# Performance work log

Measured on AMD Instinct MI355X. Metric: run time of the kernel, lower is better.

Reference implementation:

```python
import jax, jax.numpy as jnp
import numpy as np

B, IN, H, N, W, K = 32, 256, 512, 32768, 64, 8
EPS = 1e-12  # torch F.normalize eps


def setup_inputs() -> dict:
    key = jax.random.key(0)
    ks = jax.random.split(key, 16)
    inp = {
        "x": jax.random.normal(ks[0], (B, IN), jnp.float32),
        "h_prev": jax.random.normal(ks[1], (B, H), jnp.float32),
        "c_prev": jax.random.normal(ks[2], (B, H), jnp.float32),
        "M_prev": jax.random.normal(ks[3], (B, N, W), jnp.float32),
        "wr_prev": jax.random.uniform(ks[4], (B, N), jnp.float32),
        "usage_prev": jax.random.uniform(ks[5], (B, N), jnp.float32),
        "r_prev": jax.random.normal(ks[6], (B, W), jnp.float32),
        # LSTMCell params (torch layout: [4H, in] / [4H, H], gate order i,f,g,o)
        "W_ih": jax.random.normal(ks[7], (4 * H, IN + W), jnp.float32) * 0.02,
        "W_hh": jax.random.normal(ks[8], (4 * H, H), jnp.float32) * 0.02,
        "b_ih": jax.random.normal(ks[9], (4 * H,), jnp.float32) * 0.02,
        "b_hh": jax.random.normal(ks[10], (4 * H,), jnp.float32) * 0.02,
        # output_projector: hidden -> 3W + 2
        "W_proj": jax.random.normal(ks[11], (3 * W + 2, H), jnp.float32) * 0.02,
        "b_proj": jax.random.normal(ks[12], (3 * W + 2,), jnp.float32) * 0.02,
        # final_projector: hidden + W -> hidden
        "W_final": jax.random.normal(ks[13], (H, H + W), jnp.float32) * 0.02,
        "b_final": jax.random.normal(ks[14], (H,), jnp.float32) * 0.02,
    }
    return inp


def _l2norm(v, axis):
    n = jnp.sqrt(jnp.sum(v * v, axis=axis, keepdims=True))
    return v / jnp.maximum(n, EPS)


def reference(x, h_prev, c_prev, M_prev, wr_prev, usage_prev, r_prev,
              W_ih, W_hh, b_ih, b_hh, W_proj, b_proj, W_final, b_final):
    # ---- LSTM controller step ----
    lstm_in = jnp.concatenate([x, r_prev], axis=1)            # [B, IN+W]
    gates = lstm_in @ W_ih.T + b_ih + h_prev @ W_hh.T + b_hh  # [B, 4H]
    gi, gf, gg, go = jnp.split(gates, 4, axis=1)
    i = jax.nn.sigmoid(gi)
    f = jax.nn.sigmoid(gf)
    g = jnp.tanh(gg)
    o = jax.nn.sigmoid(go)
    c_curr = f * c_prev + i * g
    h_curr = o * jnp.tanh(c_curr)

    # ---- interface params ----
    params = h_curr @ W_proj.T + b_proj                       # [B, 3W+2]
    q = params[:, :W]
    a = params[:, W:2 * W]
    e = jax.nn.sigmoid(params[:, 2 * W:3 * W])
    alpha = jax.nn.sigmoid(params[:, -2:-1])                  # [B,1]
    gamma = jax.nn.sigmoid(params[:, -1:])                    # [B,1]

    # ---- sparse read: cosine sim -> topK -> scattered softmax ----
    q_n = _l2norm(q, axis=1)                                  # [B, W]
    m_n = _l2norm(M_prev, axis=2)                             # [B, N, W]
    sim = jnp.einsum('bw,bnw->bn', q_n, m_n)                  # [B, N]
    top_vals, top_idx = jax.lax.top_k(sim, K)                 # [B, K]
    sm = jax.nn.softmax(top_vals, axis=1)                     # softmax(-inf elsewhere) == 0
    b_idx = jnp.arange(sim.shape[0])[:, None]
    w_r = jnp.zeros_like(sim).at[b_idx, top_idx].set(sm)      # [B, N]
    r_curr = jnp.einsum('bn,bnw->bw', w_r, M_prev)            # [B, W]

    # ---- usage / LRU write weights ----
    usage_curr = usage_prev + 1.0
    access_mask = jnp.zeros_like(usage_curr).at[b_idx, top_idx].set(1.0)
    usage_curr = usage_curr * (1.0 - access_mask)
    lru = jnp.argmax(usage_curr, axis=1)                      # [B]
    I_U = jax.nn.one_hot(lru, usage_curr.shape[1], dtype=usage_curr.dtype)
    w_w = alpha * (gamma * wr_prev + (1.0 - gamma) * I_U)     # [B, N]

    # ---- rank-1 erase / add memory update ----
    w_w_exp = w_w[:, :, None]                                 # [B, N, 1]
    M_curr = M_prev * (1.0 - w_w_exp * e[:, None, :]) + w_w_exp * a[:, None, :]

    # ---- output ----
    y_out = jnp.concatenate([h_curr, r_curr], axis=1) @ W_final.T + b_final
    return (y_out, h_curr, c_curr, M_curr, w_r, usage_curr, r_curr)
```

## Files before the change

kernel.cpp:

```cpp
#include <hip/hip_runtime.h>
#include <math.h>

#define B_ 32
#define IN_ 256
#define H_ 512
#define N_ 32768
#define W_ 64
#define K_ 8
#define PROJ_ 194
#define NCHUNK 32
#define CROWS 1024
#define NCAND 1024

typedef float f32x4 __attribute__((ext_vector_type(4)));

#define OUT_Y  0
#define OUT_H  16384
#define OUT_C  32768
#define OUT_M  49152
#define OUT_WR 67158016
#define OUT_US 68206592
#define OUT_R  69255168

#define WS_QN    0
#define WS_AA    2048
#define WS_EE    4096
#define WS_ALPHA 6144
#define WS_GAMMA 6176
#define WS_LRU   6208
#define WS_CVAL  8192
#define WS_CIDX  40960

__device__ __forceinline__ float sigmoidf_(float v) { return 1.f / (1.f + expf(-v)); }

__global__ __launch_bounds__(256) void k_lstm(
    const float* __restrict__ x, const float* __restrict__ r_prev,
    const float* __restrict__ h_prev, const float* __restrict__ c_prev,
    const float* __restrict__ W_ih, const float* __restrict__ W_hh,
    const float* __restrict__ b_ih, const float* __restrict__ b_hh,
    float* __restrict__ h_out, float* __restrict__ c_out) {
  int wid = (blockIdx.x * blockDim.x + threadIdx.x) >> 6;
  int lane = threadIdx.x & 63;
  if (wid >= B_ * H_) return;
  int b = wid >> 9;
  int h = wid & (H_ - 1);
  float a0 = 0.f, a1 = 0.f, a2 = 0.f, a3 = 0.f;
  const float4* x4 = (const float4*)(x + b * IN_);
  const float4* r4 = (const float4*)(r_prev + b * W_);
  for (int c = lane; c < 80; c += 64) {
    float4 in4 = (c < 64) ? x4[c] : r4[c - 64];
    #pragma unroll
    for (int g = 0; g < 4; ++g) {
      float4 w4 = ((const float4*)(W_ih + (size_t)(g * H_ + h) * 320))[c];
      float d = fmaf(w4.x, in4.x, fmaf(w4.y, in4.y, fmaf(w4.z, in4.z, w4.w * in4.w)));
      if (g == 0) a0 += d; else if (g == 1) a1 += d; else if (g == 2) a2 += d; else a3 += d;
    }
  }
  const float4* h4 = (const float4*)(h_prev + b * H_);
  for (int c = lane; c < 128; c += 64) {
    float4 in4 = h4[c];
    #pragma unroll
    for (int g = 0; g < 4; ++g) {
      float4 w4 = ((const float4*)(W_hh + (size_t)(g * H_ + h) * 512))[c];
      float d = fmaf(w4.x, in4.x, fmaf(w4.y, in4.y, fmaf(w4.z, in4.z, w4.w * in4.w)));
      if (g == 0) a0 += d; else if (g == 1) a1 += d; else if (g == 2) a2 += d; else a3 += d;
    }
  }
  #pragma unroll
  for (int m = 1; m < 64; m <<= 1) {
    a0 += __shfl_xor(a0, m); a1 += __shfl_xor(a1, m);
    a2 += __shfl_xor(a2, m); a3 += __shfl_xor(a3, m);
  }
  if (lane == 0) {
    float gi = a0 + b_ih[h] + b_hh[h];
    float gf = a1 + b_ih[H_ + h] + b_hh[H_ + h];
    float gg = a2 + b_ih[2 * H_ + h] + b_hh[2 * H_ + h];
    float go = a3 + b_ih[3 * H_ + h] + b_hh[3 * H_ + h];
    float i_ = sigmoidf_(gi), f_ = sigmoidf_(gf), g_ = tanhf(gg), o_ = sigmoidf_(go);
    float cc = f_ * c_prev[b * H_ + h] + i_ * g_;
    c_out[b * H_ + h] = cc;
    h_out[b * H_ + h] = o_ * tanhf(cc);
  }
}

__global__ __launch_bounds__(256) void k_projpost(
    const float* __restrict__ h_curr, const float* __restrict__ W_proj,
    const float* __restrict__ b_proj, float* __restrict__ qn,
    float* __restrict__ aa, float* __restrict__ ee,
    float* __restrict__ alpha, float* __restrict__ gamma) {
  int b = blockIdx.x, tid = threadIdx.x;
  int wave = tid >> 6, lane = tid & 63;
  __shared__ float params[PROJ_];
  const float4* h4 = (const float4*)(h_curr + b * H_);
  float4 ha = h4[lane], hb = h4[lane + 64];
  for (int p = wave; p < PROJ_; p += 4) {
    const float4* w4p = (const float4*)(W_proj + (size_t)p * H_);
    float4 wa = w4p[lane], wb = w4p[lane + 64];
    float acc = fmaf(wa.x, ha.x, fmaf(wa.y, ha.y, fmaf(wa.z, ha.z, wa.w * ha.w)))
              + fmaf(wb.x, hb.x, fmaf(wb.y, hb.y, fmaf(wb.z, hb.z, wb.w * hb.w)));
    #pragma unroll
    for (int m = 1; m < 64; m <<= 1) acc += __shfl_xor(acc, m);
    if (lane == 0) params[p] = acc + b_proj[p];
  }
  __syncthreads();
  if (tid < W_) {
    float q = params[tid];
    float s = q * q;
    #pragma unroll
    for (int m = 1; m < 64; m <<= 1) s += __shfl_xor(s, m);
    float nrm = fmaxf(sqrtf(s), 1e-12f);
    qn[b * W_ + tid] = q / nrm;
    aa[b * W_ + tid] = params[W_ + tid];
    ee[b * W_ + tid] = sigmoidf_(params[2 * W_ + tid]);
    if (tid == 0) alpha[b] = sigmoidf_(params[192]);
    if (tid == 1) gamma[b] = sigmoidf_(params[193]);
  }
}

__global__ __launch_bounds__(256) void k_simupd(
    const float* __restrict__ M, const float* __restrict__ qn,
    const float* __restrict__ wr_prev, const float* __restrict__ aa,
    const float* __restrict__ ee, const float* __restrict__ alpha,
    const float* __restrict__ gamma, float* __restrict__ M_out,
    float* __restrict__ cval, int* __restrict__ cidx, float* __restrict__ w_r) {
  int b = blockIdx.y, chunk = blockIdx.x, tid = threadIdx.x;
  int j = tid & 15;
  __shared__ float simv[CROWS];
  f32x4 z = {0.f, 0.f, 0.f, 0.f};
  __builtin_nontemporal_store(z, (f32x4*)(w_r + (size_t)b * N_ + chunk * CROWS + tid * 4));
  const float* Mb = M + ((size_t)b * N_ + (size_t)chunk * CROWS) * W_;
  float* Ob = M_out + ((size_t)b * N_ + (size_t)chunk * CROWS) * W_;
  const float* wrb = wr_prev + (size_t)b * N_ + chunk * CROWS;
  float4 q4 = ((const float4*)(qn + b * W_))[j];
  float4 e4 = ((const float4*)(ee + b * W_))[j];
  float4 a4 = ((const float4*)(aa + b * W_))[j];
  float c0 = alpha[b] * gamma[b];
  #pragma unroll 8
  for (int it = 0; it < 64; ++it) {
    float4 m4 = *(const float4*)(Mb + (size_t)it * 1024 + tid * 4);
    int r = it * 16 + (tid >> 4);
    float ww = c0 * wrb[r];
    f32x4 o;
    o.x = fmaf(m4.x, 1.f - ww * e4.x, ww * a4.x);
    o.y = fmaf(m4.y, 1.f - ww * e4.y, ww * a4.y);
    o.z = fmaf(m4.z, 1.f - ww * e4.z, ww * a4.z);
    o.w = fmaf(m4.w, 1.f - ww * e4.w, ww * a4.w);
    __builtin_nontemporal_store(o, (f32x4*)(Ob + (size_t)it * 1024 + tid * 4));
    float dot = fmaf(m4.x, q4.x, fmaf(m4.y, q4.y, fmaf(m4.z, q4.z, m4.w * q4.w)));
    float sq  = fmaf(m4.x, m4.x, fmaf(m4.y, m4.y, fmaf(m4.z, m4.z, m4.w * m4.w)));
    #pragma unroll
    for (int m = 1; m < 16; m <<= 1) { dot += __shfl_xor(dot, m); sq += __shfl_xor(sq, m); }
    if (j == 0) simv[r] = dot / fmaxf(sqrtf(sq), 1e-12f);
  }
  __syncthreads();
  int wave = tid >> 6, lane = tid & 63;
  int rbase = wave * 256 + lane;
  float v0 = simv[rbase];
  float v1 = simv[rbase + 64];
  float v2 = simv[rbase + 128];
  float v3 = simv[rbase + 192];
  int base = chunk * CROWS + rbase;
  float myv = 0.f; int myi = 0;
  #pragma unroll
  for (int sel = 0; sel < K_; ++sel) {
    float bv = v0; int bk = 0;
    if (v1 > bv) { bv = v1; bk = 1; }
    if (v2 > bv) { bv = v2; bk = 2; }
    if (v3 > bv) { bv = v3; bk = 3; }
    int bi = base + (bk << 6);
    #pragma unroll
    for (int m = 1; m < 64; m <<= 1) {
      float ov = __shfl_xor(bv, m); int oi = __shfl_xor(bi, m);
      if (ov > bv || (ov == bv && oi < bi)) { bv = ov; bi = oi; }
    }
    if (bi == base)            v0 = -INFINITY;
    else if (bi == base + 64)  v1 = -INFINITY;
    else if (bi == base + 128) v2 = -INFINITY;
    else if (bi == base + 192) v3 = -INFINITY;
    if (lane == sel) { myv = bv; myi = bi; }
  }
  if (lane < K_) {
    size_t co = ((size_t)(b * NCHUNK + chunk) * 4 + wave) * K_ + lane;
    cval[co] = myv;
    cidx[co] = myi;
  }
}

__global__ __launch_bounds__(1024) void k_muse(
    const float* __restrict__ cval, const int* __restrict__ cidx,
    const float* __restrict__ M, const float* __restrict__ usage_prev,
    float* __restrict__ usage_out, float* __restrict__ r_out,
    float* __restrict__ w_r, int* __restrict__ lru) {
  int b = blockIdx.x, tid = threadIdx.x;
  __shared__ float wv[16]; __shared__ int wi[16];
  float v = cval[(size_t)b * NCAND + tid];
  int idx = cidx[(size_t)b * NCAND + tid];
  float topv[K_]; int topi[K_];
  #pragma unroll
  for (int sel = 0; sel < K_; ++sel) {
    float bv = v; int bi = idx;
    #pragma unroll
    for (int m = 1; m < 64; m <<= 1) {
      float ov = __shfl_xor(bv, m); int oi = __shfl_xor(bi, m);
      if (ov > bv || (ov == bv && oi < bi)) { bv = ov; bi = oi; }
    }
    if ((tid & 63) == 0) { wv[tid >> 6] = bv; wi[tid >> 6] = bi; }
    __syncthreads();
    float gv = wv[0]; int gi = wi[0];
    #pragma unroll
    for (int w = 1; w < 16; ++w) {
      float ov = wv[w]; int oi = wi[w];
      if (ov > gv || (ov == gv && oi < gi)) { gv = ov; gi = oi; }
    }
    if (idx == gi) v = -INFINITY;
    topv[sel] = gv; topi[sel] = gi;
    __syncthreads();
  }
  float mx = topv[0], ssum = 0.f, e[K_];
  #pragma unroll
  for (int k = 0; k < K_; ++k) { e[k] = expf(topv[k] - mx); ssum += e[k]; }
  #pragma unroll
  for (int k = 0; k < K_; ++k) e[k] /= ssum;
  if (tid < K_) w_r[(size_t)b * N_ + topi[tid]] = e[tid];
  if (tid < W_) {
    float acc = 0.f;
    #pragma unroll
    for (int k = 0; k < K_; ++k)
      acc += e[k] * M[((size_t)b * N_ + (size_t)topi[k]) * W_ + tid];
    r_out[b * W_ + tid] = acc;
  }
  const f32x4* up = (const f32x4*)(usage_prev + (size_t)b * N_);
  f32x4* uo = (f32x4*)(usage_out + (size_t)b * N_);
  float bu = -1.f; int bn = 0x7fffffff;
  for (int i = tid; i < N_ / 4; i += 1024) {
    f32x4 u = up[i];
    int n0 = i * 4;
    float uu[4] = {u.x + 1.f, u.y + 1.f, u.z + 1.f, u.w + 1.f};
    #pragma unroll
    for (int c = 0; c < 4; ++c) {
      int n = n0 + c;
      bool acc = false;
      #pragma unroll
      for (int k = 0; k < K_; ++k) acc |= (n == topi[k]);
      if (acc) uu[c] = 0.f;
      if (uu[c] > bu || (uu[c] == bu && n < bn)) { bu = uu[c]; bn = n; }
    }
    f32x4 w = {uu[0], uu[1], uu[2], uu[3]};
    __builtin_nontemporal_store(w, &uo[i]);
  }
  #pragma unroll
  for (int m = 1; m < 64; m <<= 1) {
    float ov = __shfl_xor(bu, m); int oi = __shfl_xor(bn, m);
    if (ov > bu || (ov == bu && oi < bn)) { bu = ov; bn = oi; }
  }
  if ((tid & 63) == 0) { wv[tid >> 6] = bu; wi[tid >> 6] = bn; }
  __syncthreads();
  if (tid == 0) {
    float gv = wv[0]; int gi = wi[0];
    #pragma unroll
    for (int w = 1; w < 16; ++w) {
      float ov = wv[w]; int oi = wi[w];
      if (ov > gv || (ov == gv && oi < gi)) { gv = ov; gi = oi; }
    }
    lru[b] = gi;
  }
}

__global__ void k_fix(
    const float* __restrict__ M, const float* __restrict__ wr_prev,
    const float* __restrict__ aa, const float* __restrict__ ee,
    const float* __restrict__ alpha, const float* __restrict__ gamma,
    const int* __restrict__ lru, float* __restrict__ M_out) {
  int b = blockIdx.x, t = threadIdx.x;
  int n = lru[b];
  float al = alpha[b], ga = gamma[b];
  float ww = al * (ga * wr_prev[(size_t)b * N_ + n] + (1.f - ga));
  float e = ee[b * W_ + t], a = aa[b * W_ + t];
  float m = M[((size_t)b * N_ + n) * W_ + t];
  M_out[((size_t)b * N_ + n) * W_ + t] = fmaf(m, 1.f - ww * e, ww * a);
}

__global__ __launch_bounds__(256) void k_yout(
    const float* __restrict__ h_curr, const float* __restrict__ r_curr,
    const float* __restrict__ W_final, const float* __restrict__ b_final,
    float* __restrict__ y) {
  int wid = (blockIdx.x * blockDim.x + threadIdx.x) >> 6;
  int lane = threadIdx.x & 63;
  if (wid >= B_ * H_) return;
  int b = wid >> 9;
  int o = wid & (H_ - 1);
  float acc = 0.f;
  const float4* h4 = (const float4*)(h_curr + b * H_);
  const float4* r4 = (const float4*)(r_curr + b * W_);
  const float4* w4p = (const float4*)(W_final + (size_t)o * 576);
  for (int c = lane; c < 144; c += 64) {
    float4 in4 = (c < 128) ? h4[c] : r4[c - 128];
    float4 w4 = w4p[c];
    acc += fmaf(w4.x, in4.x, fmaf(w4.y, in4.y, fmaf(w4.z, in4.z, w4.w * in4.w)));
  }
  #pragma unroll
  for (int m = 1; m < 64; m <<= 1) acc += __shfl_xor(acc, m);
  if (lane == 0) y[b * H_ + o] = acc + b_final[o];
}

extern "C" void kernel_launch(void* const* d_in, const int* in_sizes, int n_in,
                              void* d_out, int out_size, void* d_ws, size_t ws_size,
                              hipStream_t stream) {
  const float* x          = (const float*)d_in[0];
  const float* h_prev     = (const float*)d_in[1];
  const float* c_prev     = (const float*)d_in[2];
  const float* M_prev     = (const float*)d_in[3];
  const float* wr_prev    = (const float*)d_in[4];
  const float* usage_prev = (const float*)d_in[5];
  const float* r_prev     = (const float*)d_in[6];
  const float* W_ih       = (const float*)d_in[7];
  const float* W_hh       = (const float*)d_in[8];
  const float* b_ih       = (const float*)d_in[9];
  const float* b_hh       = (const float*)d_in[10];
  const float* W_proj     = (const float*)d_in[11];
  const float* b_proj     = (const float*)d_in[12];
  const float* W_final    = (const float*)d_in[13];
  const float* b_final    = (const float*)d_in[14];

  float* out   = (float*)d_out;
  float* y_out = out + OUT_Y;
  float* h_out = out + OUT_H;
  float* c_out = out + OUT_C;
  float* M_out = out + OUT_M;
  float* wr_out = out + OUT_WR;
  float* us_out = out + OUT_US;
  float* r_out  = out + OUT_R;

  float* ws    = (float*)d_ws;
  float* qn    = ws + WS_QN;
  float* aa    = ws + WS_AA;
  float* ee    = ws + WS_EE;
  float* alpha = ws + WS_ALPHA;
  float* gamma = ws + WS_GAMMA;
  int*   lru   = (int*)(ws + WS_LRU);
  float* cval  = ws + WS_CVAL;
  int*   cidx  = (int*)(ws + WS_CIDX);

  k_lstm<<<4096, 256, 0, stream>>>(x, r_prev, h_prev, c_prev, W_ih, W_hh, b_ih, b_hh,
                                   h_out, c_out);
  k_projpost<<<32, 256, 0, stream>>>(h_out, W_proj, b_proj, qn, aa, ee, alpha, gamma);
  dim3 sg(NCHUNK, B_);
  k_simupd<<<sg, 256, 0, stream>>>(M_prev, qn, wr_prev, aa, ee, alpha, gamma,
                                   M_out, cval, cidx, wr_out);
  k_muse<<<32, 1024, 0, stream>>>(cval, cidx, M_prev, usage_prev, us_out, r_out,
                                  wr_out, lru);
  k_fix<<<32, 64, 0, stream>>>(M_prev, wr_prev, aa, ee, alpha, gamma, lru, M_out);
  k_yout<<<4096, 256, 0, stream>>>(h_out, r_out, W_final, b_final, y_out);
}
```

Measured before the change: 189.8 us.

## Double-buffer memory loads and stage write weights in LDS for sim/update kernel

Rewrites the main streaming loop of the similarity/memory-update kernel as a software pipeline with two 8-deep register buffers, so loads of the next eight rows are issued before the current eight are processed. The per-row write weights are precomputed once into shared memory, replacing a scattered global read of wr_prev on every iteration. Launch bounds now request 4 blocks per SM. The aim is to keep more loads in flight on this bandwidth-bound kernel, at the cost of higher register pressure and an extra barrier.

```diff
diff --git a/kernel.cpp b/kernel.cpp
--- a/kernel.cpp
+++ b/kernel.cpp
@@ -117,7 +117,25 @@
   }
 }
 
-__global__ __launch_bounds__(256) void k_simupd(
+#define PROC(mm, ITER) do {                                                   \
+    int r_ = (ITER) * 16 + (tid >> 4);                                        \
+    float ww_ = wwv[r_];                                                      \
+    f32x4 o_;                                                                 \
+    o_.x = fmaf(mm.x, 1.f - ww_ * e4.x, ww_ * a4.x);                          \
+    o_.y = fmaf(mm.y, 1.f - ww_ * e4.y, ww_ * a4.y);                          \
+    o_.z = fmaf(mm.z, 1.f - ww_ * e4.z, ww_ * a4.z);                          \
+    o_.w = fmaf(mm.w, 1.f - ww_ * e4.w, ww_ * a4.w);                          \
+    __builtin_nontemporal_store(o_, &Ov[(ITER) * 256 + tid]);                 \
+    float dot_ = fmaf(mm.x, q4.x, fmaf(mm.y, q4.y, fmaf(mm.z, q4.z, mm.w * q4.w))); \
+    float sq_  = fmaf(mm.x, mm.x, fmaf(mm.y, mm.y, fmaf(mm.z, mm.z, mm.w * mm.w))); \
+    dot_ += __shfl_xor(dot_, 1);  sq_ += __shfl_xor(sq_, 1);                  \
+    dot_ += __shfl_xor(dot_, 2);  sq_ += __shfl_xor(sq_, 2);                  \
+    dot_ += __shfl_xor(dot_, 4);  sq_ += __shfl_xor(sq_, 4);                  \
+    dot_ += __shfl_xor(dot_, 8);  sq_ += __shfl_xor(sq_, 8);                  \
+    if (j == 0) simv[r_] = dot_ / fmaxf(sqrtf(sq_), 1e-12f);                  \
+  } while (0)
+
+__global__ __launch_bounds__(256, 4) void k_simupd(
     const float* __restrict__ M, const float* __restrict__ qn,
     const float* __restrict__ wr_prev, const float* __restrict__ aa,
     const float* __restrict__ ee, const float* __restrict__ alpha,
@@ -126,31 +144,34 @@
   int b = blockIdx.y, chunk = blockIdx.x, tid = threadIdx.x;
   int j = tid & 15;
   __shared__ float simv[CROWS];
+  __shared__ float wwv[CROWS];
   f32x4 z = {0.f, 0.f, 0.f, 0.f};
   __builtin_nontemporal_store(z, (f32x4*)(w_r + (size_t)b * N_ + chunk * CROWS + tid * 4));
-  const float* Mb = M + ((size_t)b * N_ + (size_t)chunk * CROWS) * W_;
-  float* Ob = M_out + ((size_t)b * N_ + (size_t)chunk * CROWS) * W_;
+  const f32x4* Mv = (const f32x4*)(M + ((size_t)b * N_ + (size_t)chunk * CROWS) * W_);
+  f32x4* Ov = (f32x4*)(M_out + ((size_t)b * N_ + (size_t)chunk * CROWS) * W_);
   const float* wrb = wr_prev + (size_t)b * N_ + chunk * CROWS;
   float4 q4 = ((const float4*)(qn + b * W_))[j];
   float4 e4 = ((const float4*)(ee + b * W_))[j];
   float4 a4 = ((const float4*)(aa + b * W_))[j];
   float c0 = alpha[b] * gamma[b];
-  #pragma unroll 8
-  for (int it = 0; it < 64; ++it) {
-    float4 m4 = *(const float4*)(Mb + (size_t)it * 1024 + tid * 4);
-    int r = it * 16 + (tid >> 4);
-    float ww = c0 * wrb[r];
-    f32x4 o;
-    o.x = fmaf(m4.x, 1.f - ww * e4.x, ww * a4.x);
-    o.y = fmaf(m4.y, 1.f - ww * e4.y, ww * a4.y);
-    o.z = fmaf(m4.z, 1.f - ww * e4.z, ww * a4.z);
-    o.w = fmaf(m4.w, 1.f - ww * e4.w, ww * a4.w);
-    __builtin_nontemporal_store(o, (f32x4*)(Ob + (size_t)it * 1024 + tid * 4));
-    float dot = fmaf(m4.x, q4.x, fmaf(m4.y, q4.y, fmaf(m4.z, q4.z, m4.w * q4.w)));
-    float sq  = fmaf(m4.x, m4.x, fmaf(m4.y, m4.y, fmaf(m4.z, m4.z, m4.w * m4.w)));
-    #pragma unroll
-    for (int m = 1; m < 16; m <<= 1) { dot += __shfl_xor(dot, m); sq += __shfl_xor(sq, m); }
-    if (j == 0) simv[r] = dot / fmaxf(sqrtf(sq), 1e-12f);
+  #pragma unroll
+  for (int i = 0; i < 4; ++i) wwv[tid + 256 * i] = c0 * wrb[tid + 256 * i];
+  __syncthreads();
+  f32x4 bufA[8], bufB[8];
+  #pragma unroll
+  for (int u = 0; u < 8; ++u) bufA[u] = Mv[u * 256 + tid];
+  #pragma unroll
+  for (int itb = 0; itb < 64; itb += 16) {
+    #pragma unroll
+    for (int u = 0; u < 8; ++u) bufB[u] = Mv[(itb + 8 + u) * 256 + tid];
+    #pragma unroll
+    for (int u = 0; u < 8; ++u) PROC(bufA[u], itb + u);
+    if (itb + 16 < 64) {
+      #pragma unroll
+      for (int u = 0; u < 8; ++u) bufA[u] = Mv[(itb + 16 + u) * 256 + tid];
+    }
+    #pragma unroll
+    for (int u = 0; u < 8; ++u) PROC(bufB[u], itb + 8 + u);
   }
   __syncthreads();
   int wave = tid >> 6, lane = tid & 63;
```

After: 180.9 us. 4.7% less time.
